# Kernel optimization log

Hardware: AMD Instinct MI355X
Metric: run time of the kernel (lower is better)

Reference implementation:

```python
import jax, jax.numpy as jnp
import numpy as np

T, H, E, K, I, S = 512, 1024, 32, 4, 512, 2048  # tokens, hidden, experts, top_k, moe_inter, shared_inter


def setup_inputs() -> dict:
    key = jax.random.key(0)
    ks = jax.random.split(key, 8)
    sc = 0.02
    return {
        "hidden_states": jax.random.normal(ks[0], (T, H), jnp.float32),
        "Wg": jax.random.normal(ks[1], (H, E + 1), jnp.float32) * sc,          # router gate + shared gate (merged)
        "W_gate": jax.random.normal(ks[2], (E, H, I), jnp.float32) * sc,        # per-expert gate proj
        "W_up": jax.random.normal(ks[3], (E, H, I), jnp.float32) * sc,          # per-expert up proj
        "W_down": jax.random.normal(ks[4], (E, I, H), jnp.float32) * sc,        # per-expert down proj
        "Ws_gate": jax.random.normal(ks[5], (H, S), jnp.float32) * sc,          # shared expert gate proj
        "Ws_up": jax.random.normal(ks[6], (H, S), jnp.float32) * sc,            # shared expert up proj
        "Ws_down": jax.random.normal(ks[7], (S, H), jnp.float32) * sc,          # shared expert down proj
    }


def reference(hidden_states, Wg, W_gate, W_up, W_down, Ws_gate, Ws_up, Ws_down):
    x = hidden_states  # [T, H]
    logits = x @ Wg                       # [T, E+1]
    router_logits = logits[:, :E]         # [T, E]
    shared_gate_logits = logits[:, E:]    # [T, 1]

    # top-k softmax routing with renormalization (renormalize=True)
    probs = jax.nn.softmax(router_logits, axis=-1)          # [T, E]
    topk_w, topk_idx = jax.lax.top_k(probs, K)               # [T, K]
    topk_w = topk_w / jnp.sum(topk_w, axis=-1, keepdims=True)
    combine = jnp.zeros((T, E), x.dtype).at[jnp.arange(T)[:, None], topk_idx].add(topk_w)  # [T, E]

    # routed experts: dense reference over all experts, combined by routing weights
    g = jnp.einsum("th,ehi->eti", x, W_gate)                 # [E, T, I]
    u = jnp.einsum("th,ehi->eti", x, W_up)                   # [E, T, I]
    h = jax.nn.silu(g) * u                                    # SiluAndMul
    y = jnp.einsum("eti,eih->eth", h, W_down)                # [E, T, H]
    routed = jnp.einsum("te,eth->th", combine, y)            # [T, H]

    # shared expert MLP + sigmoid shared-gate
    sh = (jax.nn.silu(x @ Ws_gate) * (x @ Ws_up)) @ Ws_down  # [T, H]
    shared = jax.nn.sigmoid(shared_gate_logits) * sh

    return shared + routed
```

## Files before the change

kernel.cpp:

```cpp
#include <hip/hip_runtime.h>
#include <hip/hip_bf16.h>

#define TT 512
#define HH 1024
#define EE 32
#define KK 4
#define II 512
#define SS 2048

using f32x4 = __attribute__((ext_vector_type(4))) float;
using s16x8 = __attribute__((ext_vector_type(8))) short;

__device__ __forceinline__ unsigned short f2bf(float f){
  unsigned int u = __builtin_bit_cast(unsigned int, f);
  u += 0x7fffu + ((u >> 16) & 1u);
  return (unsigned short)(u >> 16);
}

__device__ __forceinline__ uint4 cvt8(const float* f){
  uint4 v;
  v.x = (unsigned)f2bf(f[0]) | ((unsigned)f2bf(f[1])<<16);
  v.y = (unsigned)f2bf(f[2]) | ((unsigned)f2bf(f[3])<<16);
  v.z = (unsigned)f2bf(f[4]) | ((unsigned)f2bf(f[5])<<16);
  v.w = (unsigned)f2bf(f[6]) | ((unsigned)f2bf(f[7])<<16);
  return v;
}

__global__ __launch_bounds__(64) void k_router(
    const float* __restrict__ x, const float* __restrict__ Wg,
    unsigned short* __restrict__ xb, int* __restrict__ topk_idx,
    float* __restrict__ topk_w, float* __restrict__ sig_gate){
  int t = blockIdx.x; int l = threadIdx.x;
  const float* xr = x + (size_t)t * HH;
  #pragma unroll
  for(int i=0;i<HH/64;i++){
    int h = l + 64*i;
    xb[(size_t)t*HH + h] = f2bf(xr[h]);
  }
  float acc0=0.f, acc1=0.f, acc2=0.f, acc3=0.f;
  if(l < EE+1){
    const float* wcol = Wg + l;
    for(int h=0; h<HH; h+=4){
      acc0 += xr[h]   * wcol[(size_t)h*(EE+1)];
      acc1 += xr[h+1] * wcol[(size_t)(h+1)*(EE+1)];
      acc2 += xr[h+2] * wcol[(size_t)(h+2)*(EE+1)];
      acc3 += xr[h+3] * wcol[(size_t)(h+3)*(EE+1)];
    }
  }
  __shared__ float lg[EE+1];
  if(l < EE+1) lg[l] = (acc0+acc1)+(acc2+acc3);
  __syncthreads();
  if(l == 0){
    float v[EE];
    #pragma unroll
    for(int i=0;i<EE;i++) v[i]=lg[i];
    int idx[KK]; float val[KK];
    #pragma unroll
    for(int k=0;k<KK;k++){
      float m=-1e30f; int mi=0;
      for(int i=0;i<EE;i++){ if(v[i]>m){ m=v[i]; mi=i; } }
      idx[k]=mi; val[k]=m; v[mi]=-1e30f;
    }
    float mx = val[0], s=0.f; float w[KK];
    #pragma unroll
    for(int k=0;k<KK;k++){ w[k]=__expf(val[k]-mx); s+=w[k]; }
    float inv = 1.f/s;
    #pragma unroll
    for(int k=0;k<KK;k++){ topk_idx[t*KK+k]=idx[k]; topk_w[t*KK+k]=w[k]*inv; }
    sig_gate[t] = 1.f/(1.f+__expf(-lg[EE]));
  }
}

__global__ __launch_bounds__(64) void k_build(
    const int* __restrict__ topk_idx, const float* __restrict__ topk_w,
    int* __restrict__ token_list, float* __restrict__ weight_list,
    int* __restrict__ counts){
  int e = blockIdx.x; int l = threadIdx.x;
  int cnt = 0;
  for(int c=0;c<TT;c+=64){
    int t = c + l;
    int kk = -1;
    #pragma unroll
    for(int k=0;k<KK;k++) if(topk_idx[t*KK+k]==e) kk=k;
    unsigned long long b = __ballot(kk>=0);
    int pre = __popcll(b & ((1ull<<l)-1ull));
    if(kk>=0){
      token_list[e*TT + cnt + pre] = t;
      weight_list[e*TT + cnt + pre] = topk_w[t*KK+kk];
    }
    cnt += __popcll(b);
  }
  if(l==0) counts[e]=cnt;
}

template<int RG, bool DUAL>
__device__ __forceinline__ void gemm64(
    const unsigned short* A0, const unsigned short* A1, bool va,
    const float* Gp, const float* Up, int ldb, int NK,
    f32x4 (*ag)[4], f32x4 (*au)[4],
    unsigned short* As, unsigned short* Bg, unsigned short* Bu, int tid){
  const int MR = RG*64;
  const int w = tid>>6, l = tid&63;
  const int n = tid&63, kh = tid>>6, ar = tid>>2, as_ = tid&3;
  const int kt = l>>4, mm = l&15;
  uint4 av0 = make_uint4(0,0,0,0), av1 = make_uint4(0,0,0,0);
  float gv[8], uv[8];
  if(va) av0 = *reinterpret_cast<const uint4*>(A0);
  if(RG==2) av1 = *reinterpret_cast<const uint4*>(A1);
  #pragma unroll
  for(int i=0;i<8;i++) gv[i] = Gp[(size_t)i*ldb];
  if(DUAL){
    #pragma unroll
    for(int i=0;i<8;i++) uv[i] = Up[(size_t)i*ldb];
  }
  *reinterpret_cast<uint4*>(As + (size_t)ar*40 + as_*8) = av0;
  if(RG==2) *reinterpret_cast<uint4*>(As + (size_t)(64+ar)*40 + as_*8) = av1;
  *reinterpret_cast<uint4*>(Bg + (size_t)n*40 + kh*8) = cvt8(gv);
  if(DUAL) *reinterpret_cast<uint4*>(Bu + (size_t)n*40 + kh*8) = cvt8(uv);
  __syncthreads();
  for(int ks=0; ks<NK; ks++){
    const int cur = ks & 1;
    const bool more = (ks+1 < NK);
    if(more){
      av0 = make_uint4(0,0,0,0);
      if(va) av0 = *reinterpret_cast<const uint4*>(A0 + (size_t)(ks+1)*32);
      if(RG==2) av1 = *reinterpret_cast<const uint4*>(A1 + (size_t)(ks+1)*32);
      const float* g = Gp + (size_t)(ks+1)*32*ldb;
      #pragma unroll
      for(int i=0;i<8;i++) gv[i] = g[(size_t)i*ldb];
      if(DUAL){
        const float* u = Up + (size_t)(ks+1)*32*ldb;
        #pragma unroll
        for(int i=0;i<8;i++) uv[i] = u[(size_t)i*ldb];
      }
    }
    s16x8 bg_[4], bu_[4];
    #pragma unroll
    for(int c=0;c<4;c++){
      bg_[c] = *reinterpret_cast<const s16x8*>(Bg + ((size_t)cur*64 + c*16 + mm)*40 + kt*8);
      if(DUAL)
        bu_[c] = *reinterpret_cast<const s16x8*>(Bu + ((size_t)cur*64 + c*16 + mm)*40 + kt*8);
    }
    #pragma unroll
    for(int rg=0; rg<RG; rg++){
      s16x8 af = *reinterpret_cast<const s16x8*>(As + ((size_t)cur*MR + rg*64 + w*16 + mm)*40 + kt*8);
      #pragma unroll
      for(int c=0;c<4;c++){
        ag[rg][c] = __builtin_amdgcn_mfma_f32_16x16x32_bf16(af, bg_[c], ag[rg][c], 0,0,0);
        if(DUAL)
          au[rg][c] = __builtin_amdgcn_mfma_f32_16x16x32_bf16(af, bu_[c], au[rg][c], 0,0,0);
      }
    }
    if(more){
      const int nx = cur^1;
      *reinterpret_cast<uint4*>(As + ((size_t)nx*MR + ar)*40 + as_*8) = av0;
      if(RG==2) *reinterpret_cast<uint4*>(As + ((size_t)nx*MR + 64 + ar)*40 + as_*8) = av1;
      *reinterpret_cast<uint4*>(Bg + ((size_t)nx*64 + n)*40 + kh*8) = cvt8(gv);
      if(DUAL) *reinterpret_cast<uint4*>(Bu + ((size_t)nx*64 + n)*40 + kh*8) = cvt8(uv);
    }
    __syncthreads();
  }
}

__global__ __launch_bounds__(256) void k_gateup_all(
    const unsigned short* __restrict__ xb,
    const float* __restrict__ Wsg, const float* __restrict__ Wsu,
    unsigned short* __restrict__ Hs,
    const float* __restrict__ Wgate, const float* __restrict__ Wup,
    const int* __restrict__ token_list, const int* __restrict__ counts,
    unsigned short* __restrict__ hbuf){
  __shared__ unsigned short As[2*128*40];
  __shared__ unsigned short Bg[2*64*40];
  __shared__ unsigned short Bu[2*64*40];
  int tid = threadIdx.x, w = tid>>6, l = tid&63;
  int ar = tid>>2, as_ = tid&3, n = tid&63, kh = tid>>6;
  int bid = blockIdx.x;
  f32x4 zero = {0.f,0.f,0.f,0.f};
  const int NSH = (TT/128)*(SS/64);

  if(bid < NSH){
    int n0 = (bid & 31) * 64;
    int r0 = (bid >> 5) * 128;
    f32x4 ag[2][4], au[2][4];
    #pragma unroll
    for(int rg=0;rg<2;rg++)
      #pragma unroll
      for(int c=0;c<4;c++){ ag[rg][c]=zero; au[rg][c]=zero; }
    const unsigned short* A0 = xb + (size_t)(r0+ar)*HH + as_*8;
    const unsigned short* A1 = A0 + (size_t)64*HH;
    const float* Gp = Wsg + (size_t)(kh*8)*SS + n0 + n;
    const float* Up = Wsu + (size_t)(kh*8)*SS + n0 + n;
    gemm64<2,true>(A0, A1, true, Gp, Up, SS, HH/32, ag, au, As, Bg, Bu, tid);
    int mm = l&15;
    #pragma unroll
    for(int rg=0;rg<2;rg++){
      int rb = r0 + rg*64 + w*16 + (l>>4)*4;
      #pragma unroll
      for(int c=0;c<4;c++){
        #pragma unroll
        for(int j=0;j<4;j++){
          float g = ag[rg][c][j], u = au[rg][c][j];
          Hs[(size_t)(rb+j)*SS + n0 + c*16 + mm] = f2bf(g*u/(1.f+__expf(-g)));
        }
      }
    }
  } else {
    int b = bid - NSH;
    int e = b >> 3;
    int i0 = (b & 7) * 64;
    int cnt = counts[e]; if(cnt == 0) return;
    int off = 0;
    for(int i=0;i<e;i++) off += counts[i];
    const float* Bg0 = Wgate + (size_t)e*HH*II;
    const float* Bu0 = Wup   + (size_t)e*HH*II;
    for(int rt=0; rt*64<cnt; rt++){
      int nv = cnt - rt*64; if(nv > 64) nv = 64;
      const int* rows = token_list + e*TT + rt*64;
      int arow = (ar < nv) ? rows[ar] : 0;
      bool va = ar < nv;
      f32x4 ag[1][4], au[1][4];
      #pragma unroll
      for(int c=0;c<4;c++){ ag[0][c]=zero; au[0][c]=zero; }
      const unsigned short* A0 = xb + (size_t)arow*HH + as_*8;
      const float* Gp = Bg0 + (size_t)(kh*8)*II + i0 + n;
      const float* Up = Bu0 + (size_t)(kh*8)*II + i0 + n;
      gemm64<1,true>(A0, A0, va, Gp, Up, II, HH/32, ag, au, As, Bg, Bu, tid);
      int mm = l&15, rr0 = w*16 + (l>>4)*4;
      #pragma unroll
      for(int c=0;c<4;c++){
        #pragma unroll
        for(int j=0;j<4;j++){
          int rr = rr0 + j;
          if(rr < nv){
            float g = ag[0][c][j], u = au[0][c][j];
            hbuf[(size_t)(off+rt*64+rr)*II + i0 + c*16 + mm] =
                f2bf(g*u/(1.f+__expf(-g)));
          }
        }
      }
    }
  }
}

__global__ __launch_bounds__(256) void k_down_all(
    const unsigned short* __restrict__ Hsrc, const float* __restrict__ Wsd,
    const float* __restrict__ sig_gate,
    const unsigned short* __restrict__ hbuf, const float* __restrict__ Wdown,
    const int* __restrict__ token_list, const float* __restrict__ weight_list,
    const int* __restrict__ counts, float* __restrict__ out){
  __shared__ unsigned short As[2*128*40];
  __shared__ unsigned short Bs[2*64*40];
  int tid = threadIdx.x, w = tid>>6, l = tid&63;
  int ar = tid>>2, as_ = tid&3, n = tid&63, kh = tid>>6;
  int bid = blockIdx.x;
  f32x4 zero = {0.f,0.f,0.f,0.f};
  const int NSH = (TT/128)*(HH/64);

  if(bid < NSH){
    int n0 = (bid & 15) * 64;
    int r0 = (bid >> 4) * 128;
    f32x4 acc[2][4];
    #pragma unroll
    for(int rg=0;rg<2;rg++)
      #pragma unroll
      for(int c=0;c<4;c++) acc[rg][c]=zero;
    const unsigned short* A0 = Hsrc + (size_t)(r0+ar)*SS + as_*8;
    const unsigned short* A1 = A0 + (size_t)64*SS;
    const float* Bp = Wsd + (size_t)(kh*8)*HH + n0 + n;
    gemm64<2,false>(A0, A1, true, Bp, Bp, HH, SS/32, acc, acc, As, Bs, Bs, tid);
    int mm = l&15;
    #pragma unroll
    for(int rg=0;rg<2;rg++){
      int rb = r0 + rg*64 + w*16 + (l>>4)*4;
      #pragma unroll
      for(int c=0;c<4;c++){
        #pragma unroll
        for(int j=0;j<4;j++){
          atomicAdd(&out[(size_t)(rb+j)*HH + n0 + c*16 + mm],
                    sig_gate[rb+j]*acc[rg][c][j]);
        }
      }
    }
  } else {
    int b = bid - NSH;
    int e = b >> 4;
    int n0 = (b & 15) * 64;
    int cnt = counts[e]; if(cnt == 0) return;
    int off = 0;
    for(int i=0;i<e;i++) off += counts[i];
    const float* B0 = Wdown + (size_t)e*II*HH;
    for(int rt=0; rt*64<cnt; rt++){
      int nv = cnt - rt*64; if(nv > 64) nv = 64;
      bool va = ar < nv;
      f32x4 acc[1][4];
      #pragma unroll
      for(int c=0;c<4;c++) acc[0][c]=zero;
      const unsigned short* A0 = hbuf + (size_t)(off+rt*64+ar)*II + as_*8;
      const float* Bp = B0 + (size_t)(kh*8)*HH + n0 + n;
      gemm64<1,false>(A0, A0, va, Bp, Bp, HH, II/32, acc, acc, As, Bs, Bs, tid);
      int mm = l&15, rr0 = w*16 + (l>>4)*4;
      #pragma unroll
      for(int c=0;c<4;c++){
        #pragma unroll
        for(int j=0;j<4;j++){
          int rr = rr0 + j;
          if(rr < nv){
            int t = token_list[e*TT + rt*64 + rr];
            float wt = weight_list[e*TT + rt*64 + rr];
            atomicAdd(&out[(size_t)t*HH + n0 + c*16 + mm], wt*acc[0][c][j]);
          }
        }
      }
    }
  }
}

extern "C" void kernel_launch(void* const* d_in, const int* in_sizes, int n_in,
                              void* d_out, int out_size, void* d_ws, size_t ws_size,
                              hipStream_t stream) {
  const float* x     = (const float*)d_in[0];
  const float* Wg    = (const float*)d_in[1];
  const float* Wgate = (const float*)d_in[2];
  const float* Wup   = (const float*)d_in[3];
  const float* Wdown = (const float*)d_in[4];
  const float* Wsg   = (const float*)d_in[5];
  const float* Wsu   = (const float*)d_in[6];
  const float* Wsd   = (const float*)d_in[7];
  float* out = (float*)d_out;

  char* ws = (char*)d_ws;
  unsigned short* xb   = (unsigned short*)ws; ws += (size_t)TT*HH*2;
  unsigned short* Hs   = (unsigned short*)ws; ws += (size_t)TT*SS*2;
  unsigned short* hbuf = (unsigned short*)ws; ws += (size_t)(TT*KK+64)*II*2;
  int*   token_list  = (int*)ws;   ws += (size_t)EE*TT*4;
  float* weight_list = (float*)ws; ws += (size_t)EE*TT*4;
  int*   topk_idx    = (int*)ws;   ws += (size_t)TT*KK*4;
  float* topk_wq     = (float*)ws; ws += (size_t)TT*KK*4;
  int*   counts      = (int*)ws;   ws += 128;
  float* sig_gate    = (float*)ws; ws += (size_t)TT*4;

  hipMemsetAsync(d_out, 0, (size_t)TT*HH*4, stream);
  k_router<<<TT, 64, 0, stream>>>(x, Wg, xb, topk_idx, topk_wq, sig_gate);
  k_build<<<EE, 64, 0, stream>>>(topk_idx, topk_wq, token_list, weight_list, counts);
  k_gateup_all<<<(TT/128)*(SS/64) + EE*(II/64), 256, 0, stream>>>(
      xb, Wsg, Wsu, Hs, Wgate, Wup, token_list, counts, hbuf);
  k_down_all<<<(TT/128)*(HH/64) + EE*(HH/64), 256, 0, stream>>>(
      Hs, Wsd, sig_gate, hbuf, Wdown, token_list, weight_list, counts, out);
}
```

Measured before the change: 151.4 us.

## Vectorize fp32 weight loads as float4 and shrink shared-expert tiles to 64 rows

B-tile loading changes from eight strided scalar fp32 loads per thread to two float4 row loads. Each thread now converts four columns across two k-rows and writes them to LDS as packed 32-bit pairs. Shared-expert GEMM tiles also drop from 128 to 64 rows, which doubles the block count for those parts and removes the RG template. The aim is more coalesced global reads and more parallelism, at the cost of rereading each weight tile twice as often and using narrower LDS stores that may cause bank conflicts.

```diff
diff --git a/kernel.cpp b/kernel.cpp
--- a/kernel.cpp
+++ b/kernel.cpp
@@ -15,15 +15,6 @@
   unsigned int u = __builtin_bit_cast(unsigned int, f);
   u += 0x7fffu + ((u >> 16) & 1u);
   return (unsigned short)(u >> 16);
-}
-
-__device__ __forceinline__ uint4 cvt8(const float* f){
-  uint4 v;
-  v.x = (unsigned)f2bf(f[0]) | ((unsigned)f2bf(f[1])<<16);
-  v.y = (unsigned)f2bf(f[2]) | ((unsigned)f2bf(f[3])<<16);
-  v.z = (unsigned)f2bf(f[4]) | ((unsigned)f2bf(f[5])<<16);
-  v.w = (unsigned)f2bf(f[6]) | ((unsigned)f2bf(f[7])<<16);
-  return v;
 }
 
 __global__ __launch_bounds__(64) void k_router(
@@ -93,45 +84,52 @@
   if(l==0) counts[e]=cnt;
 }
 
-template<int RG, bool DUAL>
+__device__ __forceinline__ void stB(unsigned short* B, int nb, int krow,
+                                    float4 r0, float4 r1){
+  const float* a = (const float*)&r0;
+  const float* b = (const float*)&r1;
+  #pragma unroll
+  for(int j=0;j<4;j++){
+    unsigned v = (unsigned)f2bf(a[j]) | ((unsigned)f2bf(b[j]) << 16);
+    *reinterpret_cast<unsigned*>(B + (size_t)(nb+j)*40 + krow) = v;
+  }
+}
+
+template<bool DUAL>
 __device__ __forceinline__ void gemm64(
-    const unsigned short* A0, const unsigned short* A1, bool va,
+    const unsigned short* A0, bool va,
     const float* Gp, const float* Up, int ldb, int NK,
-    f32x4 (*ag)[4], f32x4 (*au)[4],
+    f32x4* ag, f32x4* au,
     unsigned short* As, unsigned short* Bg, unsigned short* Bu, int tid){
-  const int MR = RG*64;
   const int w = tid>>6, l = tid&63;
-  const int n = tid&63, kh = tid>>6, ar = tid>>2, as_ = tid&3;
+  const int ar = tid>>2, as_ = tid&3;
+  const int krow = 2*(tid>>4), nb = 4*(tid&15);
   const int kt = l>>4, mm = l&15;
-  uint4 av0 = make_uint4(0,0,0,0), av1 = make_uint4(0,0,0,0);
-  float gv[8], uv[8];
-  if(va) av0 = *reinterpret_cast<const uint4*>(A0);
-  if(RG==2) av1 = *reinterpret_cast<const uint4*>(A1);
-  #pragma unroll
-  for(int i=0;i<8;i++) gv[i] = Gp[(size_t)i*ldb];
+  uint4 av = va ? *reinterpret_cast<const uint4*>(A0) : make_uint4(0,0,0,0);
+  float4 g0 = *reinterpret_cast<const float4*>(Gp + (size_t)krow*ldb);
+  float4 g1 = *reinterpret_cast<const float4*>(Gp + (size_t)(krow+1)*ldb);
+  float4 u0, u1;
   if(DUAL){
-    #pragma unroll
-    for(int i=0;i<8;i++) uv[i] = Up[(size_t)i*ldb];
-  }
-  *reinterpret_cast<uint4*>(As + (size_t)ar*40 + as_*8) = av0;
-  if(RG==2) *reinterpret_cast<uint4*>(As + (size_t)(64+ar)*40 + as_*8) = av1;
-  *reinterpret_cast<uint4*>(Bg + (size_t)n*40 + kh*8) = cvt8(gv);
-  if(DUAL) *reinterpret_cast<uint4*>(Bu + (size_t)n*40 + kh*8) = cvt8(uv);
+    u0 = *reinterpret_cast<const float4*>(Up + (size_t)krow*ldb);
+    u1 = *reinterpret_cast<const float4*>(Up + (size_t)(krow+1)*ldb);
+  }
+  *reinterpret_cast<uint4*>(As + (size_t)ar*40 + as_*8) = av;
+  stB(Bg, nb, krow, g0, g1);
+  if(DUAL) stB(Bu, nb, krow, u0, u1);
   __syncthreads();
   for(int ks=0; ks<NK; ks++){
     const int cur = ks & 1;
     const bool more = (ks+1 < NK);
     if(more){
-      av0 = make_uint4(0,0,0,0);
-      if(va) av0 = *reinterpret_cast<const uint4*>(A0 + (size_t)(ks+1)*32);
-      if(RG==2) av1 = *reinterpret_cast<const uint4*>(A1 + (size_t)(ks+1)*32);
-      const float* g = Gp + (size_t)(ks+1)*32*ldb;
-      #pragma unroll
-      for(int i=0;i<8;i++) gv[i] = g[(size_t)i*ldb];
+      av = va ? *reinterpret_cast<const uint4*>(A0 + (size_t)(ks+1)*32)
+              : make_uint4(0,0,0,0);
+      const float* gb = Gp + (size_t)(ks+1)*32*ldb;
+      g0 = *reinterpret_cast<const float4*>(gb + (size_t)krow*ldb);
+      g1 = *reinterpret_cast<const float4*>(gb + (size_t)(krow+1)*ldb);
       if(DUAL){
-        const float* u = Up + (size_t)(ks+1)*32*ldb;
-        #pragma unroll
-        for(int i=0;i<8;i++) uv[i] = u[(size_t)i*ldb];
+        const float* ub = Up + (size_t)(ks+1)*32*ldb;
+        u0 = *reinterpret_cast<const float4*>(ub + (size_t)krow*ldb);
+        u1 = *reinterpret_cast<const float4*>(ub + (size_t)(krow+1)*ldb);
       }
     }
     s16x8 bg_[4], bu_[4];
@@ -141,22 +139,18 @@
       if(DUAL)
         bu_[c] = *reinterpret_cast<const s16x8*>(Bu + ((size_t)cur*64 + c*16 + mm)*40 + kt*8);
     }
-    #pragma unroll
-    for(int rg=0; rg<RG; rg++){
-      s16x8 af = *reinterpret_cast<const s16x8*>(As + ((size_t)cur*MR + rg*64 + w*16 + mm)*40 + kt*8);
-      #pragma unroll
-      for(int c=0;c<4;c++){
-        ag[rg][c] = __builtin_amdgcn_mfma_f32_16x16x32_bf16(af, bg_[c], ag[rg][c], 0,0,0);
-        if(DUAL)
-          au[rg][c] = __builtin_amdgcn_mfma_f32_16x16x32_bf16(af, bu_[c], au[rg][c], 0,0,0);
-      }
+    s16x8 af = *reinterpret_cast<const s16x8*>(As + ((size_t)cur*64 + w*16 + mm)*40 + kt*8);
+    #pragma unroll
+    for(int c=0;c<4;c++){
+      ag[c] = __builtin_amdgcn_mfma_f32_16x16x32_bf16(af, bg_[c], ag[c], 0,0,0);
+      if(DUAL)
+        au[c] = __builtin_amdgcn_mfma_f32_16x16x32_bf16(af, bu_[c], au[c], 0,0,0);
     }
     if(more){
       const int nx = cur^1;
-      *reinterpret_cast<uint4*>(As + ((size_t)nx*MR + ar)*40 + as_*8) = av0;
-      if(RG==2) *reinterpret_cast<uint4*>(As + ((size_t)nx*MR + 64 + ar)*40 + as_*8) = av1;
-      *reinterpret_cast<uint4*>(Bg + ((size_t)nx*64 + n)*40 + kh*8) = cvt8(gv);
-      if(DUAL) *reinterpret_cast<uint4*>(Bu + ((size_t)nx*64 + n)*40 + kh*8) = cvt8(uv);
+      *reinterpret_cast<uint4*>(As + ((size_t)nx*64 + ar)*40 + as_*8) = av;
+      stB(Bg + (size_t)nx*64*40, nb, krow, g0, g1);
+      if(DUAL) stB(Bu + (size_t)nx*64*40, nb, krow, u0, u1);
     }
     __syncthreads();
   }
@@ -169,39 +163,30 @@
     const float* __restrict__ Wgate, const float* __restrict__ Wup,
     const int* __restrict__ token_list, const int* __restrict__ counts,
     unsigned short* __restrict__ hbuf){
-  __shared__ unsigned short As[2*128*40];
+  __shared__ unsigned short As[2*64*40];
   __shared__ unsigned short Bg[2*64*40];
   __shared__ unsigned short Bu[2*64*40];
   int tid = threadIdx.x, w = tid>>6, l = tid&63;
-  int ar = tid>>2, as_ = tid&3, n = tid&63, kh = tid>>6;
+  int ar = tid>>2, as_ = tid&3, nb = 4*(tid&15);
   int bid = blockIdx.x;
   f32x4 zero = {0.f,0.f,0.f,0.f};
-  const int NSH = (TT/128)*(SS/64);
+  const int NSH = (TT/64)*(SS/64);
 
   if(bid < NSH){
     int n0 = (bid & 31) * 64;
-    int r0 = (bid >> 5) * 128;
-    f32x4 ag[2][4], au[2][4];
-    #pragma unroll
-    for(int rg=0;rg<2;rg++)
+    int r0 = (bid >> 5) * 64;
+    f32x4 ag[4]={zero,zero,zero,zero}, au[4]={zero,zero,zero,zero};
+    const unsigned short* A0 = xb + (size_t)(r0+ar)*HH + as_*8;
+    const float* Gp = Wsg + n0 + nb;
+    const float* Up = Wsu + n0 + nb;
+    gemm64<true>(A0, true, Gp, Up, SS, HH/32, ag, au, As, Bg, Bu, tid);
+    int mm = l&15, rb = r0 + w*16 + (l>>4)*4;
+    #pragma unroll
+    for(int c=0;c<4;c++){
       #pragma unroll
-      for(int c=0;c<4;c++){ ag[rg][c]=zero; au[rg][c]=zero; }
-    const unsigned short* A0 = xb + (size_t)(r0+ar)*HH + as_*8;
-    const unsigned short* A1 = A0 + (size_t)64*HH;
-    const float* Gp = Wsg + (size_t)(kh*8)*SS + n0 + n;
-    const float* Up = Wsu + (size_t)(kh*8)*SS + n0 + n;
-    gemm64<2,true>(A0, A1, true, Gp, Up, SS, HH/32, ag, au, As, Bg, Bu, tid);
-    int mm = l&15;
-    #pragma unroll
-    for(int rg=0;rg<2;rg++){
-      int rb = r0 + rg*64 + w*16 + (l>>4)*4;
-      #pragma unroll
-      for(int c=0;c<4;c++){
-        #pragma unroll
-        for(int j=0;j<4;j++){
-          float g = ag[rg][c][j], u = au[rg][c][j];
-          Hs[(size_t)(rb+j)*SS + n0 + c*16 + mm] = f2bf(g*u/(1.f+__expf(-g)));
-        }
+      for(int j=0;j<4;j++){
+        float g = ag[c][j], u = au[c][j];
+        Hs[(size_t)(rb+j)*SS + n0 + c*16 + mm] = f2bf(g*u/(1.f+__expf(-g)));
       }
     }
   } else {
@@ -211,20 +196,16 @@
     int cnt = counts[e]; if(cnt == 0) return;
     int off = 0;
     for(int i=0;i<e;i++) off += counts[i];
-    const float* Bg0 = Wgate + (size_t)e*HH*II;
-    const float* Bu0 = Wup   + (size_t)e*HH*II;
+    const float* Gp0 = Wgate + (size_t)e*HH*II + i0 + nb;
+    const float* Up0 = Wup   + (size_t)e*HH*II + i0 + nb;
     for(int rt=0; rt*64<cnt; rt++){
       int nv = cnt - rt*64; if(nv > 64) nv = 64;
       const int* rows = token_list + e*TT + rt*64;
       int arow = (ar < nv) ? rows[ar] : 0;
       bool va = ar < nv;
-      f32x4 ag[1][4], au[1][4];
-      #pragma unroll
-      for(int c=0;c<4;c++){ ag[0][c]=zero; au[0][c]=zero; }
+      f32x4 ag[4]={zero,zero,zero,zero}, au[4]={zero,zero,zero,zero};
       const unsigned short* A0 = xb + (size_t)arow*HH + as_*8;
-      const float* Gp = Bg0 + (size_t)(kh*8)*II + i0 + n;
-      const float* Up = Bu0 + (size_t)(kh*8)*II + i0 + n;
-      gemm64<1,true>(A0, A0, va, Gp, Up, II, HH/32, ag, au, As, Bg, Bu, tid);
+      gemm64<true>(A0, va, Gp0, Up0, II, HH/32, ag, au, As, Bg, Bu, tid);
       int mm = l&15, rr0 = w*16 + (l>>4)*4;
       #pragma unroll
       for(int c=0;c<4;c++){
@@ -232,7 +213,7 @@
         for(int j=0;j<4;j++){
           int rr = rr0 + j;
           if(rr < nv){
-            float g = ag[0][c][j], u = au[0][c][j];
+            float g = ag[c][j], u = au[c][j];
             hbuf[(size_t)(off+rt*64+rr)*II + i0 + c*16 + mm] =
                 f2bf(g*u/(1.f+__expf(-g)));
           }
@@ -248,37 +229,28 @@
     const unsigned short* __restrict__ hbuf, const float* __restrict__ Wdown,
     const int* __restrict__ token_list, const float* __restrict__ weight_list,
     const int* __restrict__ counts, float* __restrict__ out){
-  __shared__ unsigned short As[2*128*40];
+  __shared__ unsigned short As[2*64*40];
   __shared__ unsigned short Bs[2*64*40];
   int tid = threadIdx.x, w = tid>>6, l = tid&63;
-  int ar = tid>>2, as_ = tid&3, n = tid&63, kh = tid>>6;
+  int ar = tid>>2, as_ = tid&3, nb = 4*(tid&15);
   int bid = blockIdx.x;
   f32x4 zero = {0.f,0.f,0.f,0.f};
-  const int NSH = (TT/128)*(HH/64);
+  const int NSH = (TT/64)*(HH/64);
 
   if(bid < NSH){
     int n0 = (bid & 15) * 64;
-    int r0 = (bid >> 4) * 128;
-    f32x4 acc[2][4];
-    #pragma unroll
-    for(int rg=0;rg<2;rg++)
+    int r0 = (bid >> 4) * 64;
+    f32x4 acc[4]={zero,zero,zero,zero};
+    const unsigned short* A0 = Hsrc + (size_t)(r0+ar)*SS + as_*8;
+    const float* Bp = Wsd + n0 + nb;
+    gemm64<false>(A0, true, Bp, Bp, HH, SS/32, acc, acc, As, Bs, Bs, tid);
+    int mm = l&15, rb = r0 + w*16 + (l>>4)*4;
+    #pragma unroll
+    for(int c=0;c<4;c++){
       #pragma unroll
-      for(int c=0;c<4;c++) acc[rg][c]=zero;
-    const unsigned short* A0 = Hsrc + (size_t)(r0+ar)*SS + as_*8;
-    const unsigned short* A1 = A0 + (size_t)64*SS;
-    const float* Bp = Wsd + (size_t)(kh*8)*HH + n0 + n;
-    gemm64<2,false>(A0, A1, true, Bp, Bp, HH, SS/32, acc, acc, As, Bs, Bs, tid);
-    int mm = l&15;
-    #pragma unroll
-    for(int rg=0;rg<2;rg++){
-      int rb = r0 + rg*64 + w*16 + (l>>4)*4;
-      #pragma unroll
-      for(int c=0;c<4;c++){
-        #pragma unroll
-        for(int j=0;j<4;j++){
-          atomicAdd(&out[(size_t)(rb+j)*HH + n0 + c*16 + mm],
-                    sig_gate[rb+j]*acc[rg][c][j]);
-        }
+      for(int j=0;j<4;j++){
+        atomicAdd(&out[(size_t)(rb+j)*HH + n0 + c*16 + mm],
+                  sig_gate[rb+j]*acc[c][j]);
       }
     }
   } else {
@@ -288,16 +260,13 @@
     int cnt = counts[e]; if(cnt == 0) return;
     int off = 0;
     for(int i=0;i<e;i++) off += counts[i];
-    const float* B0 = Wdown + (size_t)e*II*HH;
+    const float* Bp = Wdown + (size_t)e*II*HH + n0 + nb;
     for(int rt=0; rt*64<cnt; rt++){
       int nv = cnt - rt*64; if(nv > 64) nv = 64;
       bool va = ar < nv;
-      f32x4 acc[1][4];
-      #pragma unroll
-      for(int c=0;c<4;c++) acc[0][c]=zero;
+      f32x4 acc[4]={zero,zero,zero,zero};
       const unsigned short* A0 = hbuf + (size_t)(off+rt*64+ar)*II + as_*8;
-      const float* Bp = B0 + (size_t)(kh*8)*HH + n0 + n;
-      gemm64<1,false>(A0, A0, va, Bp, Bp, HH, II/32, acc, acc, As, Bs, Bs, tid);
+      gemm64<false>(A0, va, Bp, Bp, HH, II/32, acc, acc, As, Bs, Bs, tid);
       int mm = l&15, rr0 = w*16 + (l>>4)*4;
       #pragma unroll
       for(int c=0;c<4;c++){
@@ -307,7 +276,7 @@
           if(rr < nv){
             int t = token_list[e*TT + rt*64 + rr];
             float wt = weight_list[e*TT + rt*64 + rr];
-            atomicAdd(&out[(size_t)t*HH + n0 + c*16 + mm], wt*acc[0][c][j]);
+            atomicAdd(&out[(size_t)t*HH + n0 + c*16 + mm], wt*acc[c][j]);
           }
         }
       }
@@ -342,8 +311,8 @@
   hipMemsetAsync(d_out, 0, (size_t)TT*HH*4, stream);
   k_router<<<TT, 64, 0, stream>>>(x, Wg, xb, topk_idx, topk_wq, sig_gate);
   k_build<<<EE, 64, 0, stream>>>(topk_idx, topk_wq, token_list, weight_list, counts);
-  k_gateup_all<<<(TT/128)*(SS/64) + EE*(II/64), 256, 0, stream>>>(
+  k_gateup_all<<<(TT/64)*(SS/64) + EE*(II/64), 256, 0, stream>>>(
       xb, Wsg, Wsu, Hs, Wgate, Wup, token_list, counts, hbuf);
-  k_down_all<<<(TT/128)*(HH/64) + EE*(HH/64), 256, 0, stream>>>(
+  k_down_all<<<(TT/64)*(HH/64) + EE*(HH/64), 256, 0, stream>>>(
       Hs, Wsd, sig_gate, hbuf, Wdown, token_list, weight_list, counts, out);
 }
```

New measurement: 151.9 us. Within noise of the previous version (+0.3%).
